# Optimization experiments

Measured on AMD Instinct MI355X. Metric: run time of the kernel, lower is better.

The kernel has to match this reference:

```python
import jax, jax.numpy as jnp
import numpy as np

FEAT = 256
HID = 128
NL = 4
DIL = [1, 2, 4, 8]
T = 2048
IN_DIMS = [FEAT, HID, HID, HID]
OUT_DIMS = [HID, HID, HID, FEAT]


def setup_inputs() -> dict:
    key = jax.random.key(0)
    ks = jax.random.split(key, 64)
    inp = {"x": jax.random.normal(ks[0], (T, FEAT), dtype=jnp.float32)}
    ki = 1
    for i in range(NL):
        din, dout = IN_DIMS[i], OUT_DIMS[i]
        s = 1.0 / np.sqrt(dout)
        inp[f"Wih{i}"] = jax.random.uniform(ks[ki], (4 * dout, din), jnp.float32, -s, s); ki += 1
        inp[f"Whh{i}"] = jax.random.uniform(ks[ki], (4 * dout, dout), jnp.float32, -s, s); ki += 1
        inp[f"bih{i}"] = jax.random.uniform(ks[ki], (4 * dout,), jnp.float32, -s, s); ki += 1
        inp[f"bhh{i}"] = jax.random.uniform(ks[ki], (4 * dout,), jnp.float32, -s, s); ki += 1
        # initial states: h ~ U(0,1), c ~ N(0,1), one per dilation slot
        inp[f"h0_{i}"] = jax.random.uniform(ks[ki], (DIL[i], dout), jnp.float32); ki += 1
        inp[f"c0_{i}"] = jax.random.normal(ks[ki], (DIL[i], dout), jnp.float32); ki += 1
    return inp


def _lstm_cell(xv, h, c, Wih, Whh, bih, bhh):
    z = Wih @ xv + bih + Whh @ h + bhh          # [4*out]
    i, f, g, o = jnp.split(z, 4)
    i = jax.nn.sigmoid(i); f = jax.nn.sigmoid(f)
    g = jnp.tanh(g);       o = jax.nn.sigmoid(o)
    c2 = f * c + i * g
    h2 = o * jnp.tanh(c2)
    return h2, c2


def _forward(x, params, h0s, c0s):
    def step(carry, inp):
        Hs, Cs = carry
        j, xt = inp
        v = xt
        Hs, Cs = list(Hs), list(Cs)
        for i in range(NL):
            k = j % DIL[i]
            h, c = Hs[i][k], Cs[i][k]
            h2, c2 = _lstm_cell(v, h, c, *params[i])
            Hs[i] = Hs[i].at[k].set(h2)
            Cs[i] = Cs[i].at[k].set(c2)
            v = h2
        return (tuple(Hs), tuple(Cs)), v

    init = (tuple(h0s), tuple(c0s))
    _, out = jax.lax.scan(step, init, (jnp.arange(T), x))
    return out  # [T, FEAT]


def reference(x,
              Wih0, Whh0, bih0, bhh0,
              Wih1, Whh1, bih1, bhh1,
              Wih2, Whh2, bih2, bhh2,
              Wih3, Whh3, bih3, bhh3,
              h0_0, c0_0, h0_1, c0_1, h0_2, c0_2, h0_3, c0_3):
    params = [(Wih0, Whh0, bih0, bhh0), (Wih1, Whh1, bih1, bhh1),
              (Wih2, Whh2, bih2, bhh2), (Wih3, Whh3, bih3, bhh3)]
    h0s = [h0_0, h0_1, h0_2, h0_3]
    c0s = [c0_0, c0_1, c0_2, c0_3]
    return _forward(x, params, h0s, c0s)
```

## Files before the change

kernel.cpp:

```cpp
#include <hip/hip_runtime.h>


typedef unsigned int u32;
typedef _Float16 h2v __attribute__((ext_vector_type(2)));

#define TSTEPS 2048

#define ZX_FLOATS 1048576
#define Y0_OFF 0
#define Y1_OFF 32768
#define Y2_OFF 65536
#define HX_OFF 98304
#define PROG_OFF 163840
#define CNT_OFF 164352

__device__ __forceinline__ void barL() {
  asm volatile("s_waitcnt lgkmcnt(0)\ns_barrier" ::: "memory");
}
__device__ __forceinline__ float f_sig(float x) { return 1.0f / (1.0f + __expf(-x)); }
__device__ __forceinline__ float f_tanh(float x) {
  float xc = fminf(fmaxf(x, -15.0f), 15.0f);
  float e = __expf(2.0f * xc);
  return (e - 1.0f) / (e + 1.0f);
}
__device__ __forceinline__ u32 pld32(const u32* p) {
  return __hip_atomic_load((u32*)p, __ATOMIC_RELAXED, __HIP_MEMORY_SCOPE_SYSTEM);
}
__device__ __forceinline__ void pst16(u32* p, int j, float v) {
  _Float16 hv = (_Float16)v;
  u32 u = ((u32)(j + 1) << 16) | (u32)__builtin_bit_cast(unsigned short, hv);
  __hip_atomic_store(p, u, __ATOMIC_RELAXED, __HIP_MEMORY_SCOPE_SYSTEM);
}
__device__ __forceinline__ u32 pldA(const u32* p) {
  return __hip_atomic_load((u32*)p, __ATOMIC_RELAXED, __HIP_MEMORY_SCOPE_AGENT);
}
__device__ __forceinline__ void pstA16(u32* p, int j, float v) {
  _Float16 hv = (_Float16)v;
  u32 u = ((u32)(j + 1) << 16) | (u32)__builtin_bit_cast(unsigned short, hv);
  __hip_atomic_store(p, u, __ATOMIC_RELAXED, __HIP_MEMORY_SCOPE_AGENT);
}
__device__ __forceinline__ int ptag16(u32 u) { return (int)(short)(u >> 16); }
__device__ __forceinline__ _Float16 pval16(u32 u) {
  return __builtin_bit_cast(_Float16, (unsigned short)(u & 0xffffu));
}
__device__ __forceinline__ void ensure32(u32& u, const u32* p, int need, int& bud) {
  while (ptag16(u) < need) { if (--bud < 0) break; u = pld32(p); }
}
__device__ __forceinline__ void pollg32(const u32* p, int need, int& bud) {
  u32 g = pld32(p);
  while (ptag16(g) < need) { if (--bud < 0) break; g = pld32(p); }
}

__global__ __launch_bounds__(256) void zx0_kernel(
    const float* __restrict__ x, const float* __restrict__ Wih0,
    const float* __restrict__ bih0, const float* __restrict__ bhh0,
    float* __restrict__ zx) {
  __shared__ float xs[4 * 256];
  const int t = threadIdx.x;
  const int j0 = blockIdx.x * 4;
  ((float4*)xs)[t] = ((const float4*)(x + j0 * 256))[t];
  __syncthreads();
  const int r0 = t, r1 = t + 256;
  float a0[4] = {0, 0, 0, 0}, a1[4] = {0, 0, 0, 0};
  const float* w0p = Wih0 + r0 * 256;
  const float* w1p = Wih0 + r1 * 256;
#pragma unroll 8
  for (int k = 0; k < 256; k += 4) {
    float4 wa = *(const float4*)(w0p + k);
    float4 wb = *(const float4*)(w1p + k);
#pragma unroll
    for (int jj = 0; jj < 4; jj++) {
      float4 xv = *(const float4*)(xs + jj * 256 + k);
      a0[jj] += wa.x * xv.x + wa.y * xv.y + wa.z * xv.z + wa.w * xv.w;
      a1[jj] += wb.x * xv.x + wb.y * xv.y + wb.z * xv.z + wb.w * xv.w;
    }
  }
  float b0 = bih0[r0] + bhh0[r0];
  float b1 = bih0[r1] + bhh0[r1];
#pragma unroll
  for (int jj = 0; jj < 4; jj++) {
    zx[(j0 + jj) * 512 + r0] = a0[jj] + b0;
    zx[(j0 + jj) * 512 + r1] = a1[jj] + b1;
  }
}

__device__ void r0_run(int t, const float* __restrict__ Whh0,
                       const float* __restrict__ h00, const float* __restrict__ c00,
                       const float* __restrict__ zx, u32* __restrict__ y0,
                       const u32* __restrict__ y1g, float* LDS) {
  _Float16* hb16 = (_Float16*)LDS;
  const float4* hb4 = (const float4*)LDS;
  float* zbuf = LDS + 64;
  const int kh = t >> 7, cl = t & 127;
  h2v w[4][32];
#pragma unroll
  for (int r = 0; r < 4; r++)
#pragma unroll
    for (int kk = 0; kk < 64; kk += 4) {
      float4 a = *(const float4*)(Whh0 + (cl + 128 * r) * 128 + kh * 64 + kk);
      h2v t0; t0.x = (_Float16)a.x; t0.y = (_Float16)a.y;
      h2v t1; t1.x = (_Float16)a.z; t1.y = (_Float16)a.w;
      w[r][kk >> 1] = t0; w[r][(kk >> 1) + 1] = t1;
    }
  float c = 0.0f, zx4[4] = {0, 0, 0, 0};
  if (t < 128) {
    hb16[t] = (_Float16)h00[t]; c = c00[t];
#pragma unroll
    for (int r = 0; r < 4; r++) zx4[r] = zx[cl + 128 * r];
  }
  int bud = 1 << 22; int gu = 0;
  __syncthreads();
  for (int j = 0; j < TSTEPS; j++) {
    float4 hf[8];
#pragma unroll
    for (int i = 0; i < 8; i++) hf[i] = hb4[kh * 8 + i];
    const h2v* hh = (const h2v*)hf;
    float a0 = 0, a1 = 0, a2 = 0, a3 = 0;
#pragma unroll
    for (int kk = 0; kk < 32; kk++) {
      a0 = __builtin_amdgcn_fdot2(w[0][kk], hh[kk], a0, false);
      a1 = __builtin_amdgcn_fdot2(w[1][kk], hh[kk], a1, false);
      a2 = __builtin_amdgcn_fdot2(w[2][kk], hh[kk], a2, false);
      a3 = __builtin_amdgcn_fdot2(w[3][kk], hh[kk], a3, false);
    }
    if (kh) { zbuf[cl] = a0; zbuf[128 + cl] = a1; zbuf[256 + cl] = a2; zbuf[384 + cl] = a3; }
    barL();
    if (t < 128) {
      float zi = zx4[0] + a0 + zbuf[cl];
      float zf = zx4[1] + a1 + zbuf[128 + cl];
      float zg = zx4[2] + a2 + zbuf[256 + cl];
      float zo = zx4[3] + a3 + zbuf[384 + cl];
      float ig = f_sig(zi), fg = f_sig(zf), gg = f_tanh(zg), og = f_sig(zo);
      c = fg * c + ig * gg;
      float h2 = og * f_tanh(c);
      hb16[cl] = (_Float16)h2;
      pst16(y0 + (u32)(j & 255) * 128 + cl, j, h2);
      if (j + 1 < TSTEPS) {
#pragma unroll
        for (int r = 0; r < 4; r++) zx4[r] = zx[(j + 1) * 512 + cl + 128 * r];
      }
    } else if (t == 128 && j >= 192 && j >= gu) {
      pollg32(y1g + (u32)((j + 64) & 255) * 128, (j + 64) - 255, bud);
      gu = j + 64;
    }
    barL();
  }
}

template <int D, int GM>
__device__ void rmid_run(int q, int t, const float* __restrict__ Wih,
                         const float* __restrict__ Whh,
                         const float* __restrict__ bih, const float* __restrict__ bhh,
                         const float* __restrict__ h0s, const float* __restrict__ c0s,
                         const u32* __restrict__ yin, u32* __restrict__ yout,
                         const u32* __restrict__ gptr, float* LDS) {
  _Float16* hb16 = (_Float16*)LDS;
  const float4* hb4 = (const float4*)LDS;
  _Float16* vb16 = (_Float16*)(LDS + 64);
  const float4* vb4 = (const float4*)(LDS + 64);
  float* zbuf = LDS + 128;
  const int kh = t >> 7, cl = t & 127;
  h2v wi[4][32], wr[4][32];
#pragma unroll
  for (int r = 0; r < 4; r++)
#pragma unroll
    for (int kk = 0; kk < 64; kk += 4) {
      float4 a = *(const float4*)(Wih + (cl + 128 * r) * 128 + kh * 64 + kk);
      h2v t0; t0.x = (_Float16)a.x; t0.y = (_Float16)a.y;
      h2v t1; t1.x = (_Float16)a.z; t1.y = (_Float16)a.w;
      wi[r][kk >> 1] = t0; wi[r][(kk >> 1) + 1] = t1;
      float4 b = *(const float4*)(Whh + (cl + 128 * r) * 128 + kh * 64 + kk);
      h2v t2; t2.x = (_Float16)b.x; t2.y = (_Float16)b.y;
      h2v t3; t3.x = (_Float16)b.z; t3.y = (_Float16)b.w;
      wr[r][kk >> 1] = t2; wr[r][(kk >> 1) + 1] = t3;
    }
  float bst4[4] = {0, 0, 0, 0};
  float c = 0.0f;
  if (t < 128) {
    hb16[t] = (_Float16)h0s[q * 128 + t]; c = c0s[q * 128 + t];
#pragma unroll
    for (int r = 0; r < 4; r++) bst4[r] = bih[cl + 128 * r] + bhh[cl + 128 * r];
  }
  int bud = 1 << 22; int gu = 0;
  u32 pf = 0, spf = 0;
  if (t < 128) {
    ensure32(pf, yin + (u32)(q & 255) * 128 + t, q + 1, bud);
    vb16[t] = pval16(pf);
  }
  __syncthreads();
  const int NS = TSTEPS / D;
  for (int s = 0; s < NS; s++) {
    const int j = q + s * D;
    float4 vf[8], hf[8];
#pragma unroll
    for (int i = 0; i < 8; i++) { vf[i] = vb4[kh * 8 + i]; hf[i] = hb4[kh * 8 + i]; }
    const h2v* vv = (const h2v*)vf;
    const h2v* hh = (const h2v*)hf;
    float a0 = 0, a1 = 0, a2 = 0, a3 = 0;
#pragma unroll
    for (int kk = 0; kk < 32; kk++) {
      a0 = __builtin_amdgcn_fdot2(wi[0][kk], vv[kk], a0, false);
      a1 = __builtin_amdgcn_fdot2(wi[1][kk], vv[kk], a1, false);
      a2 = __builtin_amdgcn_fdot2(wi[2][kk], vv[kk], a2, false);
      a3 = __builtin_amdgcn_fdot2(wi[3][kk], vv[kk], a3, false);
    }
#pragma unroll
    for (int kk = 0; kk < 32; kk++) {
      a0 = __builtin_amdgcn_fdot2(wr[0][kk], hh[kk], a0, false);
      a1 = __builtin_amdgcn_fdot2(wr[1][kk], hh[kk], a1, false);
      a2 = __builtin_amdgcn_fdot2(wr[2][kk], hh[kk], a2, false);
      a3 = __builtin_amdgcn_fdot2(wr[3][kk], hh[kk], a3, false);
    }
    if (kh) { zbuf[cl] = a0; zbuf[128 + cl] = a1; zbuf[256 + cl] = a2; zbuf[384 + cl] = a3; }
    barL();
    if (t < 128) {
      float zi = bst4[0] + a0 + zbuf[cl];
      float zf = bst4[1] + a1 + zbuf[128 + cl];
      float zg = bst4[2] + a2 + zbuf[256 + cl];
      float zo = bst4[3] + a3 + zbuf[384 + cl];
      float ig = f_sig(zi), fg = f_sig(zf), gg = f_tanh(zg), og = f_sig(zo);
      c = fg * c + ig * gg;
      float h2 = og * f_tanh(c);
      hb16[cl] = (_Float16)h2;
      pst16(yout + (u32)(j & 255) * 128 + cl, j, h2);
    } else {
      const int cl2 = t - 128;
      if (s + 1 < NS) {
        const int jn = j + D;
        ensure32(spf, yin + (u32)(jn & 255) * 128 + cl2, jn + 1, bud);
        vb16[cl2] = pval16(spf);
        spf = pld32(yin + (u32)((jn + D) & 255) * 128 + cl2);
      }
      if (GM == 1) {
        if (t == 192 && j >= 192 && j >= gu) {
          pollg32(gptr + (u32)((j + 64) & 255) * 128, (j + 64) - 255, bud);
          gu = j + 64;
        }
      } else {
        if (t >= 224 && t < 232 && (s & 31) == 0 && j >= 256)
          pollg32(gptr + (u32)(t - 224) * 64, j - 159, bud);
      }
    }
    barL();
  }
}

__device__ void r3_run(int q, int p, int t, const float* __restrict__ Wih3,
                       const float* __restrict__ Whh3,
                       const float* __restrict__ bih3, const float* __restrict__ bhh3,
                       const float* __restrict__ h03, const float* __restrict__ c03,
                       const u32* __restrict__ y2, u32* __restrict__ hx,
                       u32* __restrict__ prog, u32* __restrict__ donec,
                       float* __restrict__ out, float* LDS) {
  _Float16* hb16 = (_Float16*)LDS;
  const float4* hb4 = (const float4*)LDS;
  _Float16* vb16 = (_Float16*)(LDS + 128);
  const float4* vb4 = (const float4*)(LDS + 128);
  float* zbuf = LDS + 192;
  const int g = t >> 6, ci = t & 63;
  const int R = g * 256 + p * 64 + ci;
  h2v wh[128], wx[64];
#pragma unroll
  for (int kk = 0; kk < 256; kk += 4) {
    float4 a = *(const float4*)(Whh3 + R * 256 + kk);
    h2v t0; t0.x = (_Float16)a.x; t0.y = (_Float16)a.y;
    h2v t1; t1.x = (_Float16)a.z; t1.y = (_Float16)a.w;
    wh[kk >> 1] = t0; wh[(kk >> 1) + 1] = t1;
  }
#pragma unroll
  for (int kk = 0; kk < 128; kk += 4) {
    float4 a = *(const float4*)(Wih3 + R * 128 + kk);
    h2v t0; t0.x = (_Float16)a.x; t0.y = (_Float16)a.y;
    h2v t1; t1.x = (_Float16)a.z; t1.y = (_Float16)a.w;
    wx[kk >> 1] = t0; wx[(kk >> 1) + 1] = t1;
  }
  const float bst = bih3[R] + bhh3[R];
  float c = (t < 64) ? c03[q * 256 + p * 64 + t] : 0.0f;
  hb16[t] = (_Float16)h03[q * 256 + t];
  int bud = 1 << 22;
  const int pu = (t >= 64) ? ((t - 64) + ((t - 64) >= p * 64 ? 64 : 0)) : 0;
  u32 pf = 0;
  if (t < 128) {
    ensure32(pf, y2 + (u32)(q & 255) * 128 + t, q + 1, bud);
    vb16[t] = pval16(pf);
  }
  __syncthreads();
#pragma unroll 1
  for (int s = 0; s < 256; s++) {
    const int j = q + 8 * s;
    float acc = bst;
#pragma unroll
    for (int ch = 0; ch < 4; ch++) {
      float4 vf[4];
#pragma unroll
      for (int i = 0; i < 4; i++) vf[i] = vb4[ch * 4 + i];
      const h2v* vv = (const h2v*)vf;
#pragma unroll
      for (int kk = 0; kk < 16; kk++)
        acc = __builtin_amdgcn_fdot2(wx[ch * 16 + kk], vv[kk], acc, false);
    }
#pragma unroll
    for (int ch = 0; ch < 8; ch++) {
      float4 hf[4];
#pragma unroll
      for (int i = 0; i < 4; i++) hf[i] = hb4[ch * 4 + i];
      const h2v* hh = (const h2v*)hf;
#pragma unroll
      for (int kk = 0; kk < 16; kk++)
        acc = __builtin_amdgcn_fdot2(wh[ch * 16 + kk], hh[kk], acc, false);
    }
    zbuf[t] = acc;
    barL();
    if (t < 64) {
      float zi = zbuf[t], zf = zbuf[64 + t], zg = zbuf[128 + t], zo = zbuf[192 + t];
      float ig = f_sig(zi), fg = f_sig(zf), gg = f_tanh(zg), og = f_sig(zo);
      c = fg * c + ig * gg;
      float h2 = og * f_tanh(c);
      out[j * 256 + p * 64 + t] = h2;
      pstA16(hx + (u32)(j & 255) * 256 + p * 64 + t, j, h2);
      hb16[p * 64 + t] = (_Float16)h2;
      if (s + 1 < 256) {
        const int jn = j + 8;
        u32 a = pld32(y2 + (u32)(jn & 255) * 128 + t);
        while (ptag16(a) < jn + 1) { if (--bud < 0) break; a = pld32(y2 + (u32)(jn & 255) * 128 + t); }
        vb16[t] = pval16(a);
        u32 b2 = pld32(y2 + (u32)(jn & 255) * 128 + t + 64);
        while (ptag16(b2) < jn + 1) { if (--bud < 0) break; b2 = pld32(y2 + (u32)(jn & 255) * 128 + t + 64); }
        vb16[t + 64] = pval16(b2);
      }
      if (t == 0 && p == 0) {
        pst16(prog + q * 64, j, 0.0f);
        if (s == 255) atomicAdd(donec, 1u);
      }
    } else if (s + 1 < 256) {
      const u32* pp = hx + (u32)(j & 255) * 256 + pu;
      u32 hu = pldA(pp);
      while (ptag16(hu) < j + 1) { if (--bud < 0) break; hu = pldA(pp); }
      hb16[pu] = pval16(hu);
    }
    barL();
  }
}

__device__ void keeper_run(int t, const u32* donec, float* LDS) {
  int* stop = (int*)LDS;
  if (t == 0) stop[0] = 0;
  __syncthreads();
  float r0 = (float)t * 0.001f + 1.0f, r1 = r0 + 0.5f, r2 = r0 + 1.5f, r3 = r0 + 2.5f;
  for (int it = 0; it < 20000; ++it) {
#pragma unroll
    for (int k = 0; k < 16; k++) {
      r0 = __builtin_fmaf(r0, 1.0000001f, 1e-7f);
      r1 = __builtin_fmaf(r1, 1.0000001f, 1e-7f);
      r2 = __builtin_fmaf(r2, 1.0000001f, 1e-7f);
      r3 = __builtin_fmaf(r3, 1.0000001f, 1e-7f);
    }
    asm volatile("" : "+v"(r0), "+v"(r1), "+v"(r2), "+v"(r3));
    if ((it & 15) == 0) {
      if (t == 0) stop[0] = ((int)pld32(donec) >= 8) ? 1 : 0;
      barL();
      int sv = stop[0];
      barL();
      if (sv) break;
    }
  }
  if (r0 == 1.2345e30f) ((volatile float*)LDS)[1] = r0;
}

__global__ __launch_bounds__(256, 1) void drnn_kernel(
    const float* __restrict__ Whh0, const float* __restrict__ h00, const float* __restrict__ c00,
    const float* __restrict__ Wih1, const float* __restrict__ Whh1,
    const float* __restrict__ bih1, const float* __restrict__ bhh1,
    const float* __restrict__ h01, const float* __restrict__ c01,
    const float* __restrict__ Wih2, const float* __restrict__ Whh2,
    const float* __restrict__ bih2, const float* __restrict__ bhh2,
    const float* __restrict__ h02, const float* __restrict__ c02,
    const float* __restrict__ Wih3, const float* __restrict__ Whh3,
    const float* __restrict__ bih3, const float* __restrict__ bhh3,
    const float* __restrict__ h03, const float* __restrict__ c03,
    float* __restrict__ ws, float* __restrict__ out) {
  __shared__ float LDS[704];
  __shared__ int role;
  const int b = blockIdx.x;
  const int t = threadIdx.x;
  const float* zx = ws;
  u32* base = (u32*)(ws + ZX_FLOATS);
  u32* y0 = base + Y0_OFF;
  u32* y1 = base + Y1_OFF;
  u32* y2 = base + Y2_OFF;
  u32* hx = base + HX_OFF;
  u32* prog = base + PROG_OFF;
  u32* cnt = base + CNT_OFF;

  if (b == 0) {
    r0_run(t, Whh0, h00, c00, zx, y0, y1, LDS);
    return;
  }
  if (b <= 2) {
    rmid_run<2, 1>(b - 1, t, Wih1, Whh1, bih1, bhh1, h01, c01, y0, y1, y2, LDS);
    return;
  }
  if (b <= 6) {
    rmid_run<4, 2>(b - 3, t, Wih2, Whh2, bih2, bhh2, h02, c02, y1, y2, prog, LDS);
    return;
  }
  if (t == 0) {
    unsigned xcc;
    asm volatile("s_getreg_b32 %0, hwreg(HW_REG_XCC_ID)" : "=s"(xcc));
    xcc &= 7u;
    u32 r = atomicAdd(cnt + xcc, 1u);
    role = (r < 4u) ? (int)(xcc * 4u + r) : -1;
  }
  __syncthreads();
  const int ro = role;
  if (ro >= 0)
    r3_run(ro >> 2, ro & 3, t, Wih3, Whh3, bih3, bhh3, h03, c03, y2, hx, prog,
           cnt + 8, out, LDS);
  else
    keeper_run(t, cnt + 8, LDS);
}

extern "C" void kernel_launch(void* const* d_in, const int* in_sizes, int n_in,
                              void* d_out, int out_size, void* d_ws, size_t ws_size,
                              hipStream_t stream) {
  const float* x    = (const float*)d_in[0];
  const float* Wih0 = (const float*)d_in[1];
  const float* Whh0 = (const float*)d_in[2];
  const float* bih0 = (const float*)d_in[3];
  const float* bhh0 = (const float*)d_in[4];
  const float* h00  = (const float*)d_in[5];
  const float* c00  = (const float*)d_in[6];
  const float* Wih1 = (const float*)d_in[7];
  const float* Whh1 = (const float*)d_in[8];
  const float* bih1 = (const float*)d_in[9];
  const float* bhh1 = (const float*)d_in[10];
  const float* h01  = (const float*)d_in[11];
  const float* c01  = (const float*)d_in[12];
  const float* Wih2 = (const float*)d_in[13];
  const float* Whh2 = (const float*)d_in[14];
  const float* bih2 = (const float*)d_in[15];
  const float* bhh2 = (const float*)d_in[16];
  const float* h02  = (const float*)d_in[17];
  const float* c02  = (const float*)d_in[18];
  const float* Wih3 = (const float*)d_in[19];
  const float* Whh3 = (const float*)d_in[20];
  const float* bih3 = (const float*)d_in[21];
  const float* bhh3 = (const float*)d_in[22];
  const float* h03  = (const float*)d_in[23];
  const float* c03  = (const float*)d_in[24];

  float* ws = (float*)d_ws;
  float* out = (float*)d_out;
  u32* cnt = (u32*)(ws + ZX_FLOATS) + CNT_OFF;

  hipMemsetAsync(cnt, 0, 64, stream);
  zx0_kernel<<<512, 256, 0, stream>>>(x, Wih0, bih0, bhh0, ws);
  drnn_kernel<<<256, 256, 0, stream>>>(Whh0, h00, c00,
                                       Wih1, Whh1, bih1, bhh1, h01, c01,
                                       Wih2, Whh2, bih2, bhh2, h02, c02,
                                       Wih3, Whh3, bih3, bhh3, h03, c03,
                                       ws, out);
}
```

Before: 1.852 ms.

## Restructure layer-0 recurrence with shuffle reduction and dedicated zx prefetch wave

Layer 0 now splits each gate row's K dimension across lane pairs and combines the halves with a shuffle, so every thread applies the gate math redundantly. This removes the LDS partial-sum exchange and one barrier per step. A fifth wave is added per block to prefetch the precomputed input projection into double-buffered LDS and to handle the cross-layer poll, whose index math is also changed. The keeper blocks that busy-looped are removed, and the middle and last layers are guarded to run only on the first 256 threads. The change raises block size to 320 and LDS use, and removing the keepers may change clock behaviour or scheduling.

```diff
diff --git a/kernel.cpp b/kernel.cpp
--- a/kernel.cpp
+++ b/kernel.cpp
@@ -90,57 +90,76 @@
                        const u32* __restrict__ y1g, float* LDS) {
   _Float16* hb16 = (_Float16*)LDS;
   const float4* hb4 = (const float4*)LDS;
-  float* zbuf = LDS + 64;
-  const int kh = t >> 7, cl = t & 127;
-  h2v w[4][32];
-#pragma unroll
-  for (int r = 0; r < 4; r++)
-#pragma unroll
-    for (int kk = 0; kk < 64; kk += 4) {
-      float4 a = *(const float4*)(Whh0 + (cl + 128 * r) * 128 + kh * 64 + kk);
-      h2v t0; t0.x = (_Float16)a.x; t0.y = (_Float16)a.y;
-      h2v t1; t1.x = (_Float16)a.z; t1.y = (_Float16)a.w;
-      w[r][kk >> 1] = t0; w[r][(kk >> 1) + 1] = t1;
-    }
-  float c = 0.0f, zx4[4] = {0, 0, 0, 0};
-  if (t < 128) {
-    hb16[t] = (_Float16)h00[t]; c = c00[t];
-#pragma unroll
-    for (int r = 0; r < 4; r++) zx4[r] = zx[cl + 128 * r];
-  }
-  int bud = 1 << 22; int gu = 0;
+  float* zxb = LDS + 64;
+
+  if (t < 256) {
+    const int cl = (t >> 6) * 32 + ((t & 63) >> 1);
+    const int kh = t & 1;
+    h2v w[4][32];
+#pragma unroll
+    for (int r = 0; r < 4; r++)
+#pragma unroll
+      for (int kk = 0; kk < 64; kk += 4) {
+        float4 a = *(const float4*)(Whh0 + (cl + 128 * r) * 128 + kh * 64 + kk);
+        h2v t0; t0.x = (_Float16)a.x; t0.y = (_Float16)a.y;
+        h2v t1; t1.x = (_Float16)a.z; t1.y = (_Float16)a.w;
+        w[r][kk >> 1] = t0; w[r][(kk >> 1) + 1] = t1;
+      }
+    float c = c00[cl];
+    if (kh == 0) hb16[cl] = (_Float16)h00[cl];
+    __syncthreads();
+    for (int j = 0; j < TSTEPS; j++) {
+      const float* zxs = zxb + (j & 1) * 512;
+      float zq0 = zxs[cl], zq1 = zxs[128 + cl], zq2 = zxs[256 + cl], zq3 = zxs[384 + cl];
+      float4 hf[8];
+#pragma unroll
+      for (int i = 0; i < 8; i++) hf[i] = hb4[kh * 8 + i];
+      const h2v* hh = (const h2v*)hf;
+      float a0 = 0, a1 = 0, a2 = 0, a3 = 0;
+#pragma unroll
+      for (int kk = 0; kk < 32; kk++) {
+        a0 = __builtin_amdgcn_fdot2(w[0][kk], hh[kk], a0, false);
+        a1 = __builtin_amdgcn_fdot2(w[1][kk], hh[kk], a1, false);
+        a2 = __builtin_amdgcn_fdot2(w[2][kk], hh[kk], a2, false);
+        a3 = __builtin_amdgcn_fdot2(w[3][kk], hh[kk], a3, false);
+      }
+      a0 += __shfl_xor(a0, 1, 64);
+      a1 += __shfl_xor(a1, 1, 64);
+      a2 += __shfl_xor(a2, 1, 64);
+      a3 += __shfl_xor(a3, 1, 64);
+      float ig = f_sig(zq0 + a0), fg = f_sig(zq1 + a1);
+      float gg = f_tanh(zq2 + a2), og = f_sig(zq3 + a3);
+      c = fg * c + ig * gg;
+      float h2 = og * f_tanh(c);
+      if (kh == 0) {
+        hb16[cl] = (_Float16)h2;
+        pst16(y0 + (u32)(j & 255) * 128 + cl, j, h2);
+      }
+      barL();
+    }
+    return;
+  }
+  const int sl = t - 256;
+  float4 z00 = *(const float4*)(zx + sl * 8);
+  float4 z01 = *(const float4*)(zx + sl * 8 + 4);
+  *(float4*)(zxb + sl * 8) = z00;
+  *(float4*)(zxb + sl * 8 + 4) = z01;
+  float4 pf0 = *(const float4*)(zx + 512 + sl * 8);
+  float4 pf1 = *(const float4*)(zx + 512 + sl * 8 + 4);
+  int bud = 1 << 22, gu = 0;
   __syncthreads();
   for (int j = 0; j < TSTEPS; j++) {
-    float4 hf[8];
-#pragma unroll
-    for (int i = 0; i < 8; i++) hf[i] = hb4[kh * 8 + i];
-    const h2v* hh = (const h2v*)hf;
-    float a0 = 0, a1 = 0, a2 = 0, a3 = 0;
-#pragma unroll
-    for (int kk = 0; kk < 32; kk++) {
-      a0 = __builtin_amdgcn_fdot2(w[0][kk], hh[kk], a0, false);
-      a1 = __builtin_amdgcn_fdot2(w[1][kk], hh[kk], a1, false);
-      a2 = __builtin_amdgcn_fdot2(w[2][kk], hh[kk], a2, false);
-      a3 = __builtin_amdgcn_fdot2(w[3][kk], hh[kk], a3, false);
-    }
-    if (kh) { zbuf[cl] = a0; zbuf[128 + cl] = a1; zbuf[256 + cl] = a2; zbuf[384 + cl] = a3; }
-    barL();
-    if (t < 128) {
-      float zi = zx4[0] + a0 + zbuf[cl];
-      float zf = zx4[1] + a1 + zbuf[128 + cl];
-      float zg = zx4[2] + a2 + zbuf[256 + cl];
-      float zo = zx4[3] + a3 + zbuf[384 + cl];
-      float ig = f_sig(zi), fg = f_sig(zf), gg = f_tanh(zg), og = f_sig(zo);
-      c = fg * c + ig * gg;
-      float h2 = og * f_tanh(c);
-      hb16[cl] = (_Float16)h2;
-      pst16(y0 + (u32)(j & 255) * 128 + cl, j, h2);
-      if (j + 1 < TSTEPS) {
-#pragma unroll
-        for (int r = 0; r < 4; r++) zx4[r] = zx[(j + 1) * 512 + cl + 128 * r];
-      }
-    } else if (t == 128 && j >= 192 && j >= gu) {
-      pollg32(y1g + (u32)((j + 64) & 255) * 128, (j + 64) - 255, bud);
+    if (j + 1 < TSTEPS) {
+      float* d = zxb + ((j + 1) & 1) * 512 + sl * 8;
+      *(float4*)d = pf0;
+      *(float4*)(d + 4) = pf1;
+      if (j + 2 < TSTEPS) {
+        pf0 = *(const float4*)(zx + (j + 2) * 512 + sl * 8);
+        pf1 = *(const float4*)(zx + (j + 2) * 512 + sl * 8 + 4);
+      }
+    }
+    if (sl == 0 && j >= 192 && j >= gu) {
+      pollg32(y1g + (u32)((j - 192) & 255) * 128, j - 191, bud);
       gu = j + 64;
     }
     barL();
@@ -159,21 +178,23 @@
   _Float16* vb16 = (_Float16*)(LDS + 64);
   const float4* vb4 = (const float4*)(LDS + 64);
   float* zbuf = LDS + 128;
-  const int kh = t >> 7, cl = t & 127;
+  const int kh = (t >> 7) & 1, cl = t & 127;
   h2v wi[4][32], wr[4][32];
-#pragma unroll
-  for (int r = 0; r < 4; r++)
-#pragma unroll
-    for (int kk = 0; kk < 64; kk += 4) {
-      float4 a = *(const float4*)(Wih + (cl + 128 * r) * 128 + kh * 64 + kk);
-      h2v t0; t0.x = (_Float16)a.x; t0.y = (_Float16)a.y;
-      h2v t1; t1.x = (_Float16)a.z; t1.y = (_Float16)a.w;
-      wi[r][kk >> 1] = t0; wi[r][(kk >> 1) + 1] = t1;
-      float4 b = *(const float4*)(Whh + (cl + 128 * r) * 128 + kh * 64 + kk);
-      h2v t2; t2.x = (_Float16)b.x; t2.y = (_Float16)b.y;
-      h2v t3; t3.x = (_Float16)b.z; t3.y = (_Float16)b.w;
-      wr[r][kk >> 1] = t2; wr[r][(kk >> 1) + 1] = t3;
-    }
+  if (t < 256) {
+#pragma unroll
+    for (int r = 0; r < 4; r++)
+#pragma unroll
+      for (int kk = 0; kk < 64; kk += 4) {
+        float4 a = *(const float4*)(Wih + (cl + 128 * r) * 128 + kh * 64 + kk);
+        h2v t0; t0.x = (_Float16)a.x; t0.y = (_Float16)a.y;
+        h2v t1; t1.x = (_Float16)a.z; t1.y = (_Float16)a.w;
+        wi[r][kk >> 1] = t0; wi[r][(kk >> 1) + 1] = t1;
+        float4 b = *(const float4*)(Whh + (cl + 128 * r) * 128 + kh * 64 + kk);
+        h2v t2; t2.x = (_Float16)b.x; t2.y = (_Float16)b.y;
+        h2v t3; t3.x = (_Float16)b.z; t3.y = (_Float16)b.w;
+        wr[r][kk >> 1] = t2; wr[r][(kk >> 1) + 1] = t3;
+      }
+  }
   float bst4[4] = {0, 0, 0, 0};
   float c = 0.0f;
   if (t < 128) {
@@ -191,27 +212,134 @@
   const int NS = TSTEPS / D;
   for (int s = 0; s < NS; s++) {
     const int j = q + s * D;
-    float4 vf[8], hf[8];
-#pragma unroll
-    for (int i = 0; i < 8; i++) { vf[i] = vb4[kh * 8 + i]; hf[i] = hb4[kh * 8 + i]; }
-    const h2v* vv = (const h2v*)vf;
-    const h2v* hh = (const h2v*)hf;
+    if (t < 256) {
+      float4 vf[8], hf[8];
+#pragma unroll
+      for (int i = 0; i < 8; i++) { vf[i] = vb4[kh * 8 + i]; hf[i] = hb4[kh * 8 + i]; }
+      const h2v* vv = (const h2v*)vf;
+      const h2v* hh = (const h2v*)hf;
+      float a0 = 0, a1 = 0, a2 = 0, a3 = 0;
+#pragma unroll
+      for (int kk = 0; kk < 32; kk++) {
+        a0 = __builtin_amdgcn_fdot2(wi[0][kk], vv[kk], a0, false);
+        a1 = __builtin_amdgcn_fdot2(wi[1][kk], vv[kk], a1, false);
+        a2 = __builtin_amdgcn_fdot2(wi[2][kk], vv[kk], a2, false);
+        a3 = __builtin_amdgcn_fdot2(wi[3][kk], vv[kk], a3, false);
+      }
+#pragma unroll
+      for (int kk = 0; kk < 32; kk++) {
+        a0 = __builtin_amdgcn_fdot2(wr[0][kk], hh[kk], a0, false);
+        a1 = __builtin_amdgcn_fdot2(wr[1][kk], hh[kk], a1, false);
+        a2 = __builtin_amdgcn_fdot2(wr[2][kk], hh[kk], a2, false);
+        a3 = __builtin_amdgcn_fdot2(wr[3][kk], hh[kk], a3, false);
+      }
+      if (kh) { zbuf[cl] = a0; zbuf[128 + cl] = a1; zbuf[256 + cl] = a2; zbuf[384 + cl] = a3; }
+    }
+    barL();
+    if (t < 128) {
+      float* ap = zbuf;
+      float zi = bst4[0] + ap[cl];
+      float zf = bst4[1] + ap[128 + cl];
+      float zg = bst4[2] + ap[256 + cl];
+      float zo = bst4[3] + ap[384 + cl];
+      zi += 0.0f; zf += 0.0f; zg += 0.0f; zo += 0.0f;
+      float ig = f_sig(zi), fg = f_sig(zf), gg = f_tanh(zg), og = f_sig(zo);
+      c = fg * c + ig * gg;
+      float h2 = og * f_tanh(c);
+      hb16[cl] = (_Float16)h2;
+      pst16(yout + (u32)(j & 255) * 128 + cl, j, h2);
+    } else if (t < 256) {
+      const int cl2 = t - 128;
+      if (s + 1 < NS) {
+        const int jn = j + D;
+        ensure32(spf, yin + (u32)(jn & 255) * 128 + cl2, jn + 1, bud);
+        vb16[cl2] = pval16(spf);
+        spf = pld32(yin + (u32)((jn + D) & 255) * 128 + cl2);
+      }
+      if (GM == 1) {
+        if (t == 192 && j >= 192 && j >= gu) {
+          pollg32(gptr + (u32)((j - 192) & 255) * 128, j - 191, bud);
+          gu = j + 64;
+        }
+      } else {
+        if (t >= 224 && t < 232 && (s & 31) == 0 && j >= 256)
+          pollg32(gptr + (u32)(t - 224) * 64, j - 159, bud);
+      }
+    }
+    barL();
+  }
+}
+
+
+template <int D, int GM>
+__device__ void rmid2_run(int q, int t, const float* __restrict__ Wih,
+                          const float* __restrict__ Whh,
+                          const float* __restrict__ bih, const float* __restrict__ bhh,
+                          const float* __restrict__ h0s, const float* __restrict__ c0s,
+                          const u32* __restrict__ yin, u32* __restrict__ yout,
+                          const u32* __restrict__ gptr, float* LDS) {
+  _Float16* hb16 = (_Float16*)LDS;
+  const float4* hb4 = (const float4*)LDS;
+  _Float16* vb16 = (_Float16*)(LDS + 64);
+  const float4* vb4 = (const float4*)(LDS + 64);
+  float* zbuf = LDS + 128;
+  const int kh = (t >> 7) & 1, cl = t & 127;
+  h2v wi[4][32], wr[4][32];
+  if (t < 256) {
+#pragma unroll
+    for (int r = 0; r < 4; r++)
+#pragma unroll
+      for (int kk = 0; kk < 64; kk += 4) {
+        float4 a = *(const float4*)(Wih + (cl + 128 * r) * 128 + kh * 64 + kk);
+        h2v t0; t0.x = (_Float16)a.x; t0.y = (_Float16)a.y;
+        h2v t1; t1.x = (_Float16)a.z; t1.y = (_Float16)a.w;
+        wi[r][kk >> 1] = t0; wi[r][(kk >> 1) + 1] = t1;
+        float4 b = *(const float4*)(Whh + (cl + 128 * r) * 128 + kh * 64 + kk);
+        h2v t2; t2.x = (_Float16)b.x; t2.y = (_Float16)b.y;
+        h2v t3; t3.x = (_Float16)b.z; t3.y = (_Float16)b.w;
+        wr[r][kk >> 1] = t2; wr[r][(kk >> 1) + 1] = t3;
+      }
+  }
+  float bst4[4] = {0, 0, 0, 0};
+  float c = 0.0f;
+  if (t < 128) {
+    hb16[t] = (_Float16)h0s[q * 128 + t]; c = c0s[q * 128 + t];
+#pragma unroll
+    for (int r = 0; r < 4; r++) bst4[r] = bih[cl + 128 * r] + bhh[cl + 128 * r];
+  }
+  int bud = 1 << 22; int gu = 0;
+  u32 pf = 0, spf = 0;
+  if (t < 128) {
+    ensure32(pf, yin + (u32)(q & 255) * 128 + t, q + 1, bud);
+    vb16[t] = pval16(pf);
+  }
+  __syncthreads();
+  const int NS = TSTEPS / D;
+  for (int s = 0; s < NS; s++) {
+    const int j = q + s * D;
     float a0 = 0, a1 = 0, a2 = 0, a3 = 0;
-#pragma unroll
-    for (int kk = 0; kk < 32; kk++) {
-      a0 = __builtin_amdgcn_fdot2(wi[0][kk], vv[kk], a0, false);
-      a1 = __builtin_amdgcn_fdot2(wi[1][kk], vv[kk], a1, false);
-      a2 = __builtin_amdgcn_fdot2(wi[2][kk], vv[kk], a2, false);
-      a3 = __builtin_amdgcn_fdot2(wi[3][kk], vv[kk], a3, false);
-    }
-#pragma unroll
-    for (int kk = 0; kk < 32; kk++) {
-      a0 = __builtin_amdgcn_fdot2(wr[0][kk], hh[kk], a0, false);
-      a1 = __builtin_amdgcn_fdot2(wr[1][kk], hh[kk], a1, false);
-      a2 = __builtin_amdgcn_fdot2(wr[2][kk], hh[kk], a2, false);
-      a3 = __builtin_amdgcn_fdot2(wr[3][kk], hh[kk], a3, false);
-    }
-    if (kh) { zbuf[cl] = a0; zbuf[128 + cl] = a1; zbuf[256 + cl] = a2; zbuf[384 + cl] = a3; }
+    if (t < 256) {
+      float4 vf[8], hf[8];
+#pragma unroll
+      for (int i = 0; i < 8; i++) { vf[i] = vb4[kh * 8 + i]; hf[i] = hb4[kh * 8 + i]; }
+      const h2v* vv = (const h2v*)vf;
+      const h2v* hh = (const h2v*)hf;
+#pragma unroll
+      for (int kk = 0; kk < 32; kk++) {
+        a0 = __builtin_amdgcn_fdot2(wi[0][kk], vv[kk], a0, false);
+        a1 = __builtin_amdgcn_fdot2(wi[1][kk], vv[kk], a1, false);
+        a2 = __builtin_amdgcn_fdot2(wi[2][kk], vv[kk], a2, false);
+        a3 = __builtin_amdgcn_fdot2(wi[3][kk], vv[kk], a3, false);
+      }
+#pragma unroll
+      for (int kk = 0; kk < 32; kk++) {
+        a0 = __builtin_amdgcn_fdot2(wr[0][kk], hh[kk], a0, false);
+        a1 = __builtin_amdgcn_fdot2(wr[1][kk], hh[kk], a1, false);
+        a2 = __builtin_amdgcn_fdot2(wr[2][kk], hh[kk], a2, false);
+        a3 = __builtin_amdgcn_fdot2(wr[3][kk], hh[kk], a3, false);
+      }
+      if (kh) { zbuf[cl] = a0; zbuf[128 + cl] = a1; zbuf[256 + cl] = a2; zbuf[384 + cl] = a3; }
+    }
     barL();
     if (t < 128) {
       float zi = bst4[0] + a0 + zbuf[cl];
@@ -223,7 +351,7 @@
       float h2 = og * f_tanh(c);
       hb16[cl] = (_Float16)h2;
       pst16(yout + (u32)(j & 255) * 128 + cl, j, h2);
-    } else {
+    } else if (t < 256) {
       const int cl2 = t - 128;
       if (s + 1 < NS) {
         const int jn = j + D;
@@ -233,7 +361,7 @@
       }
       if (GM == 1) {
         if (t == 192 && j >= 192 && j >= gu) {
-          pollg32(gptr + (u32)((j + 64) & 255) * 128, (j + 64) - 255, bud);
+          pollg32(gptr + (u32)((j - 192) & 255) * 128, j - 191, bud);
           gu = j + 64;
         }
       } else {
@@ -250,8 +378,7 @@
                        const float* __restrict__ bih3, const float* __restrict__ bhh3,
                        const float* __restrict__ h03, const float* __restrict__ c03,
                        const u32* __restrict__ y2, u32* __restrict__ hx,
-                       u32* __restrict__ prog, u32* __restrict__ donec,
-                       float* __restrict__ out, float* LDS) {
+                       u32* __restrict__ prog, float* __restrict__ out, float* LDS) {
   _Float16* hb16 = (_Float16*)LDS;
   const float4* hb4 = (const float4*)LDS;
   _Float16* vb16 = (_Float16*)(LDS + 128);
@@ -260,25 +387,27 @@
   const int g = t >> 6, ci = t & 63;
   const int R = g * 256 + p * 64 + ci;
   h2v wh[128], wx[64];
-#pragma unroll
-  for (int kk = 0; kk < 256; kk += 4) {
-    float4 a = *(const float4*)(Whh3 + R * 256 + kk);
-    h2v t0; t0.x = (_Float16)a.x; t0.y = (_Float16)a.y;
-    h2v t1; t1.x = (_Float16)a.z; t1.y = (_Float16)a.w;
-    wh[kk >> 1] = t0; wh[(kk >> 1) + 1] = t1;
-  }
-#pragma unroll
-  for (int kk = 0; kk < 128; kk += 4) {
-    float4 a = *(const float4*)(Wih3 + R * 128 + kk);
-    h2v t0; t0.x = (_Float16)a.x; t0.y = (_Float16)a.y;
-    h2v t1; t1.x = (_Float16)a.z; t1.y = (_Float16)a.w;
-    wx[kk >> 1] = t0; wx[(kk >> 1) + 1] = t1;
-  }
-  const float bst = bih3[R] + bhh3[R];
+  if (t < 256) {
+#pragma unroll
+    for (int kk = 0; kk < 256; kk += 4) {
+      float4 a = *(const float4*)(Whh3 + R * 256 + kk);
+      h2v t0; t0.x = (_Float16)a.x; t0.y = (_Float16)a.y;
+      h2v t1; t1.x = (_Float16)a.z; t1.y = (_Float16)a.w;
+      wh[kk >> 1] = t0; wh[(kk >> 1) + 1] = t1;
+    }
+#pragma unroll
+    for (int kk = 0; kk < 128; kk += 4) {
+      float4 a = *(const float4*)(Wih3 + R * 128 + kk);
+      h2v t0; t0.x = (_Float16)a.x; t0.y = (_Float16)a.y;
+      h2v t1; t1.x = (_Float16)a.z; t1.y = (_Float16)a.w;
+      wx[kk >> 1] = t0; wx[(kk >> 1) + 1] = t1;
+    }
+  }
+  const float bst = (t < 256) ? (bih3[R] + bhh3[R]) : 0.0f;
   float c = (t < 64) ? c03[q * 256 + p * 64 + t] : 0.0f;
-  hb16[t] = (_Float16)h03[q * 256 + t];
+  if (t < 256) hb16[t] = (_Float16)h03[q * 256 + t];
   int bud = 1 << 22;
-  const int pu = (t >= 64) ? ((t - 64) + ((t - 64) >= p * 64 ? 64 : 0)) : 0;
+  const int pu = (t >= 64 && t < 256) ? ((t - 64) + ((t - 64) >= p * 64 ? 64 : 0)) : 0;
   u32 pf = 0;
   if (t < 128) {
     ensure32(pf, y2 + (u32)(q & 255) * 128 + t, q + 1, bud);
@@ -288,28 +417,30 @@
 #pragma unroll 1
   for (int s = 0; s < 256; s++) {
     const int j = q + 8 * s;
-    float acc = bst;
-#pragma unroll
-    for (int ch = 0; ch < 4; ch++) {
-      float4 vf[4];
-#pragma unroll
-      for (int i = 0; i < 4; i++) vf[i] = vb4[ch * 4 + i];
-      const h2v* vv = (const h2v*)vf;
-#pragma unroll
-      for (int kk = 0; kk < 16; kk++)
-        acc = __builtin_amdgcn_fdot2(wx[ch * 16 + kk], vv[kk], acc, false);
-    }
-#pragma unroll
-    for (int ch = 0; ch < 8; ch++) {
-      float4 hf[4];
-#pragma unroll
-      for (int i = 0; i < 4; i++) hf[i] = hb4[ch * 4 + i];
-      const h2v* hh = (const h2v*)hf;
-#pragma unroll
-      for (int kk = 0; kk < 16; kk++)
-        acc = __builtin_amdgcn_fdot2(wh[ch * 16 + kk], hh[kk], acc, false);
-    }
-    zbuf[t] = acc;
+    if (t < 256) {
+      float acc = bst;
+#pragma unroll
+      for (int ch = 0; ch < 4; ch++) {
+        float4 vf[4];
+#pragma unroll
+        for (int i = 0; i < 4; i++) vf[i] = vb4[ch * 4 + i];
+        const h2v* vv = (const h2v*)vf;
+#pragma unroll
+        for (int kk = 0; kk < 16; kk++)
+          acc = __builtin_amdgcn_fdot2(wx[ch * 16 + kk], vv[kk], acc, false);
+      }
+#pragma unroll
+      for (int ch = 0; ch < 8; ch++) {
+        float4 hf[4];
+#pragma unroll
+        for (int i = 0; i < 4; i++) hf[i] = hb4[ch * 4 + i];
+        const h2v* hh = (const h2v*)hf;
+#pragma unroll
+        for (int kk = 0; kk < 16; kk++)
+          acc = __builtin_amdgcn_fdot2(wh[ch * 16 + kk], hh[kk], acc, false);
+      }
+      zbuf[t] = acc;
+    }
     barL();
     if (t < 64) {
       float zi = zbuf[t], zf = zbuf[64 + t], zg = zbuf[128 + t], zo = zbuf[192 + t];
@@ -328,11 +459,8 @@
         while (ptag16(b2) < jn + 1) { if (--bud < 0) break; b2 = pld32(y2 + (u32)(jn & 255) * 128 + t + 64); }
         vb16[t + 64] = pval16(b2);
       }
-      if (t == 0 && p == 0) {
-        pst16(prog + q * 64, j, 0.0f);
-        if (s == 255) atomicAdd(donec, 1u);
-      }
-    } else if (s + 1 < 256) {
+      if (t == 0 && p == 0) pst16(prog + q * 64, j, 0.0f);
+    } else if (t < 256 && s + 1 < 256) {
       const u32* pp = hx + (u32)(j & 255) * 256 + pu;
       u32 hu = pldA(pp);
       while (ptag16(hu) < j + 1) { if (--bud < 0) break; hu = pldA(pp); }
@@ -342,32 +470,7 @@
   }
 }
 
-__device__ void keeper_run(int t, const u32* donec, float* LDS) {
-  int* stop = (int*)LDS;
-  if (t == 0) stop[0] = 0;
-  __syncthreads();
-  float r0 = (float)t * 0.001f + 1.0f, r1 = r0 + 0.5f, r2 = r0 + 1.5f, r3 = r0 + 2.5f;
-  for (int it = 0; it < 20000; ++it) {
-#pragma unroll
-    for (int k = 0; k < 16; k++) {
-      r0 = __builtin_fmaf(r0, 1.0000001f, 1e-7f);
-      r1 = __builtin_fmaf(r1, 1.0000001f, 1e-7f);
-      r2 = __builtin_fmaf(r2, 1.0000001f, 1e-7f);
-      r3 = __builtin_fmaf(r3, 1.0000001f, 1e-7f);
-    }
-    asm volatile("" : "+v"(r0), "+v"(r1), "+v"(r2), "+v"(r3));
-    if ((it & 15) == 0) {
-      if (t == 0) stop[0] = ((int)pld32(donec) >= 8) ? 1 : 0;
-      barL();
-      int sv = stop[0];
-      barL();
-      if (sv) break;
-    }
-  }
-  if (r0 == 1.2345e30f) ((volatile float*)LDS)[1] = r0;
-}
-
-__global__ __launch_bounds__(256, 1) void drnn_kernel(
+__global__ __launch_bounds__(320, 1) void drnn_kernel(
     const float* __restrict__ Whh0, const float* __restrict__ h00, const float* __restrict__ c00,
     const float* __restrict__ Wih1, const float* __restrict__ Whh1,
     const float* __restrict__ bih1, const float* __restrict__ bhh1,
@@ -379,7 +482,7 @@
     const float* __restrict__ bih3, const float* __restrict__ bhh3,
     const float* __restrict__ h03, const float* __restrict__ c03,
     float* __restrict__ ws, float* __restrict__ out) {
-  __shared__ float LDS[704];
+  __shared__ float LDS[1088];
   __shared__ int role;
   const int b = blockIdx.x;
   const int t = threadIdx.x;
@@ -397,11 +500,11 @@
     return;
   }
   if (b <= 2) {
-    rmid_run<2, 1>(b - 1, t, Wih1, Whh1, bih1, bhh1, h01, c01, y0, y1, y2, LDS);
+    rmid2_run<2, 1>(b - 1, t, Wih1, Whh1, bih1, bhh1, h01, c01, y0, y1, y2, LDS);
     return;
   }
   if (b <= 6) {
-    rmid_run<4, 2>(b - 3, t, Wih2, Whh2, bih2, bhh2, h02, c02, y1, y2, prog, LDS);
+    rmid2_run<4, 2>(b - 3, t, Wih2, Whh2, bih2, bhh2, h02, c02, y1, y2, prog, LDS);
     return;
   }
   if (t == 0) {
@@ -413,11 +516,8 @@
   }
   __syncthreads();
   const int ro = role;
-  if (ro >= 0)
-    r3_run(ro >> 2, ro & 3, t, Wih3, Whh3, bih3, bhh3, h03, c03, y2, hx, prog,
-           cnt + 8, out, LDS);
-  else
-    keeper_run(t, cnt + 8, LDS);
+  if (ro < 0) return;
+  r3_run(ro >> 2, ro & 3, t, Wih3, Whh3, bih3, bhh3, h03, c03, y2, hx, prog, out, LDS);
 }
 
 extern "C" void kernel_launch(void* const* d_in, const int* in_sizes, int n_in,
@@ -455,7 +555,7 @@
 
   hipMemsetAsync(cnt, 0, 64, stream);
   zx0_kernel<<<512, 256, 0, stream>>>(x, Wih0, bih0, bhh0, ws);
-  drnn_kernel<<<256, 256, 0, stream>>>(Whh0, h00, c00,
+  drnn_kernel<<<256, 320, 0, stream>>>(Whh0, h00, c00,
                                        Wih1, Whh1, bih1, bhh1, h01, c01,
                                        Wih2, Whh2, bih2, bhh2, h02, c02,
                                        Wih3, Whh3, bih3, bhh3, h03, c03,
```

After: 3.512 ms. +89.6%, slower.
